# Kernel optimization log

Hardware: AMD Instinct MI355X
Metric: run time of the kernel (lower is better)

## Reference

```python
import math
import jax, jax.numpy as jnp
import numpy as np

N_HEADS = 12
D_EMBED = 768
BATCH = 2
SEQ = 2048


def setup_inputs() -> dict:
    key = jax.random.key(0)
    ks = jax.random.split(key, 5)
    scale = 0.02
    return {
        "x": jax.random.normal(ks[0], (BATCH, SEQ, D_EMBED), dtype=jnp.float32),
        "w_in": jax.random.normal(ks[1], (D_EMBED, 3 * D_EMBED), dtype=jnp.float32) * scale,
        "b_in": jax.random.normal(ks[2], (3 * D_EMBED,), dtype=jnp.float32) * scale,
        "w_out": jax.random.normal(ks[3], (D_EMBED, D_EMBED), dtype=jnp.float32) * scale,
        "b_out": jax.random.normal(ks[4], (D_EMBED,), dtype=jnp.float32) * scale,
    }


def reference(x, w_in, b_in, w_out, b_out):
    # x: [B, S, D]
    B, S, D = x.shape
    H = N_HEADS
    dh = D // H
    # Fused QKV projection: [B, S, 3D]
    qkv = x @ w_in + b_in
    q, k, v = jnp.split(qkv, 3, axis=-1)
    # [B, S, D] -> [B, H, S, dh]
    def to_heads(t):
        return t.reshape(B, S, H, dh).transpose(0, 2, 1, 3)
    q, k, v = to_heads(q), to_heads(k), to_heads(v)
    # Scaled dot-product attention (non-causal, masked=False default)
    scale = 1.0 / math.sqrt(dh)
    scores = jnp.einsum("bhqd,bhkd->bhqk", q, k) * scale  # [B, H, S, S]
    probs = jax.nn.softmax(scores, axis=-1)
    out = jnp.einsum("bhqk,bhkd->bhqd", probs, v)  # [B, H, S, dh]
    # Merge heads: [B, S, D]
    out = out.transpose(0, 2, 1, 3).reshape(B, S, D)
    return out @ w_out + b_out
```

## Files before the change

kernel.cpp:

```cpp
#include <hip/hip_runtime.h>
#include <stdint.h>

#define B_   2
#define S_   2048
#define D_   768
#define H_   12
#define DH_  64
#define N3_  2304
#define M_   4096

typedef __attribute__((ext_vector_type(8))) short    bf16x8;
typedef __attribute__((ext_vector_type(4))) float    f32x4;
typedef __attribute__((ext_vector_type(4))) int      i32x4;
typedef __attribute__((ext_vector_type(4))) unsigned short u16x4;
typedef _Float16 f16x4 __attribute__((ext_vector_type(4)));
typedef __fp16   h16x2 __attribute__((ext_vector_type(2)));

#define KSCALE 0.18033688011112042f

__device__ inline unsigned short f2bf(float f) {
    union { float f; unsigned u; } v; v.f = f;
    unsigned r = v.u + 0x7FFFu + ((v.u >> 16) & 1u);
    return (unsigned short)(r >> 16);
}

__device__ inline void async_copy16(const void* g, void* l) {
    __builtin_amdgcn_global_load_lds((const __attribute__((address_space(1))) void*)g,
                                     (__attribute__((address_space(3))) void*)l, 16, 0, 0);
}

__global__ void cvt_bf16(const float* __restrict__ in, unsigned short* __restrict__ out, int n4) {
    int i = blockIdx.x * blockDim.x + threadIdx.x;
    if (i >= n4) return;
    f32x4 v = *(const f32x4*)(in + (size_t)i * 4);
    u16x4 o;
    o.x = f2bf(v.x); o.y = f2bf(v.y); o.z = f2bf(v.z); o.w = f2bf(v.w);
    *(u16x4*)(out + (size_t)i * 4) = o;
}

__global__ void transpose_bf16(const float* __restrict__ in, unsigned short* __restrict__ out,
                               int R, int C) {
    __shared__ unsigned short t[32][33];
    int c0 = blockIdx.x * 32, r0 = blockIdx.y * 32;
    int tx = threadIdx.x, ty = threadIdx.y;
#pragma unroll
    for (int j = 0; j < 4; j++)
        t[ty + j * 8][tx] = f2bf(in[(size_t)(r0 + ty + j * 8) * C + c0 + tx]);
    __syncthreads();
#pragma unroll
    for (int j = 0; j < 4; j++)
        out[(size_t)(c0 + ty + j * 8) * R + r0 + tx] = t[tx][ty + j * 8];
}

__global__ void vtrans(const unsigned short* __restrict__ V, unsigned short* __restrict__ Vt) {
    __shared__ unsigned short t[64 * 65];
    const int bid = blockIdx.x;
    const int bh  = bid >> 5;
    const int s0  = (bid & 31) * 64;
    const int tid = threadIdx.x;
    const unsigned short* src = V  + (size_t)bh * S_ * DH_ + (size_t)s0 * DH_;
    unsigned short*       dst = Vt + (size_t)bh * DH_ * S_ + s0;
#pragma unroll
    for (int p = 0; p < 2; p++) {
        int c = p * 256 + tid;
        int s = c >> 3, dc = c & 7;
        i32x4 v = *(const i32x4*)&src[s * 64 + dc * 8];
        const unsigned short* e = (const unsigned short*)&v;
#pragma unroll
        for (int j = 0; j < 8; j++) t[(dc * 8 + j) * 65 + s] = e[j];
    }
    __syncthreads();
#pragma unroll
    for (int p = 0; p < 2; p++) {
        int c = p * 256 + tid;
        int d = c >> 3, sc = c & 7;
        unsigned short tmp[8];
#pragma unroll
        for (int j = 0; j < 8; j++) tmp[j] = t[d * 65 + sc * 8 + j];
        *(i32x4*)&dst[(size_t)d * S_ + sc * 8] = *(const i32x4*)tmp;
    }
}

template <int MODE>
__global__ __launch_bounds__(256) void gemm_bf16(
    const unsigned short* __restrict__ A,
    const unsigned short* __restrict__ Bt,
    const float* __restrict__ bias,
    void* __restrict__ Cout,
    unsigned short* __restrict__ Vnat,
    int M, int N, int K)
{
    __shared__ __align__(16) short Al[128 * 32];
    __shared__ __align__(16) short Bl[128 * 32];

    const int tid  = threadIdx.x;
    const int w    = tid >> 6;
    const int lane = tid & 63;
    const int r    = lane & 15;
    const int quad = lane >> 4;
    const int m0   = blockIdx.y * 128;
    const int n0   = blockIdx.x * 128;
    const int wm   = (w & 1) * 64;
    const int wn   = (w >> 1) * 64;

    f32x4 acc[4][4];
#pragma unroll
    for (int i = 0; i < 4; i++)
#pragma unroll
        for (int j = 0; j < 4; j++) acc[i][j] = f32x4{0.f, 0.f, 0.f, 0.f};

    const int c0 = tid, c1 = tid + 256;
    const size_t ga0 = (size_t)(m0 + (c0 >> 2)) * K + (c0 & 3) * 8;
    const size_t ga1 = (size_t)(m0 + (c1 >> 2)) * K + (c1 & 3) * 8;
    const size_t gb0 = (size_t)(n0 + (c0 >> 2)) * K + (c0 & 3) * 8;
    const size_t gb1 = (size_t)(n0 + (c1 >> 2)) * K + (c1 & 3) * 8;
    short* lA0 = &Al[(0 * 256 + w * 64) * 8];
    short* lA1 = &Al[(1 * 256 + w * 64) * 8];
    short* lB0 = &Bl[(0 * 256 + w * 64) * 8];
    short* lB1 = &Bl[(1 * 256 + w * 64) * 8];

    for (int k0 = 0; k0 < K; k0 += 32) {
        __syncthreads();
        async_copy16(A  + ga0 + k0, lA0);
        async_copy16(A  + ga1 + k0, lA1);
        async_copy16(Bt + gb0 + k0, lB0);
        async_copy16(Bt + gb1 + k0, lB1);
        __syncthreads();

        bf16x8 af[4], bf[4];
#pragma unroll
        for (int mi = 0; mi < 4; mi++)
            af[mi] = *(const bf16x8*)&Al[(wm + mi * 16 + r) * 32 + quad * 8];
#pragma unroll
        for (int ni = 0; ni < 4; ni++)
            bf[ni] = *(const bf16x8*)&Bl[(wn + ni * 16 + r) * 32 + quad * 8];
#pragma unroll
        for (int mi = 0; mi < 4; mi++)
#pragma unroll
            for (int ni = 0; ni < 4; ni++)
                acc[mi][ni] = __builtin_amdgcn_mfma_f32_16x16x32_bf16(
                    af[mi], bf[ni], acc[mi][ni], 0, 0, 0);
    }

    if (MODE == 0) {
        unsigned short* Q = (unsigned short*)Cout;
        const size_t one = (size_t)B_ * H_ * S_ * DH_;
#pragma unroll
        for (int ni = 0; ni < 4; ni++) {
            int col  = n0 + wn + ni * 16 + r;
            float bv = bias[col];
            int part = col / 768;
            int cc   = col - part * 768;
            int h    = cc >> 6;
            int d    = cc & 63;
            float scl = (part == 1) ? KSCALE : 1.0f;
            unsigned short* dst = (part == 2) ? Vnat : (Q + (size_t)part * one);
#pragma unroll
            for (int mi = 0; mi < 4; mi++) {
#pragma unroll
                for (int i = 0; i < 4; i++) {
                    int row = m0 + wm + mi * 16 + quad * 4 + i;
                    int b   = row >> 11;
                    int s   = row & 2047;
                    float v = (acc[mi][ni][i] + bv) * scl;
                    unsigned short bits;
                    if (part == 2) {
                        union { _Float16 h; unsigned short s; } cv;
                        cv.h = (_Float16)v;
                        bits = cv.s;
                    } else {
                        bits = f2bf(v);
                    }
                    dst[(((size_t)(b * H_ + h)) * S_ + s) * DH_ + d] = bits;
                }
            }
        }
    } else {
        float* Cf = (float*)Cout;
#pragma unroll
        for (int ni = 0; ni < 4; ni++) {
            int col  = n0 + wn + ni * 16 + r;
            float bv = bias[col];
#pragma unroll
            for (int mi = 0; mi < 4; mi++) {
#pragma unroll
                for (int i = 0; i < 4; i++) {
                    int row = m0 + wm + mi * 16 + quad * 4 + i;
                    Cf[(size_t)row * N + col] = acc[mi][ni][i] + bv;
                }
            }
        }
    }
}

__global__ __launch_bounds__(256) void attn_kernel(
    const unsigned short* __restrict__ Q,
    const unsigned short* __restrict__ K,
    const unsigned short* __restrict__ Vt,
    unsigned short* __restrict__ Out)
{
    __shared__ __align__(16) short Kl[64 * 64];
    __shared__ __align__(16) short Vl[64 * 64];

    const int tid  = threadIdx.x;
    const int w    = tid >> 6;
    const int lane = tid & 63;
    const int r    = lane & 15;
    const int quad = lane >> 4;
    const int xk   = r & 7;
    const int bid  = blockIdx.x;
    const int bh   = bid % 24;
    const int qb   = bid / 24;
    const int b    = bh / H_;
    const int h    = bh - b * H_;
    const size_t baseQK = (size_t)bh * S_ * DH_;
    const size_t baseV  = (size_t)bh * DH_ * S_;
    const int q0   = qb * 128;

    bf16x8 qf[2][2];
#pragma unroll
    for (int qt = 0; qt < 2; qt++) {
        const unsigned short* qp =
            Q + baseQK + (size_t)(q0 + w * 32 + qt * 16 + r) * DH_ + quad * 8;
        qf[qt][0] = *(const bf16x8*)(qp);
        qf[qt][1] = *(const bf16x8*)(qp + 32);
    }

    f32x4 o[2][4];
    f32x4 lacc[2];
#pragma unroll
    for (int qt = 0; qt < 2; qt++) {
        lacc[qt] = f32x4{0.f, 0.f, 0.f, 0.f};
#pragma unroll
        for (int nb = 0; nb < 4; nb++) o[qt][nb] = f32x4{0.f, 0.f, 0.f, 0.f};
    }

    const f16x4 ONES = {(_Float16)1.f, (_Float16)1.f, (_Float16)1.f, (_Float16)1.f};

    const int srw = tid >> 3, schk = tid & 7;
    const unsigned short* kg = K  + baseQK + tid * 8;
    const unsigned short* vg = Vt + baseV + (size_t)srw * S_ + schk * 8;
    const int lb = srw * 64 + (schk ^ (srw & 7)) * 8;

    i32x4 kreg[2], vreg[2];
    kreg[0] = *(const i32x4*)(kg);
    kreg[1] = *(const i32x4*)(kg + 2048);
    vreg[0] = *(const i32x4*)(vg);
    vreg[1] = *(const i32x4*)(vg + 32 * S_);

    for (int kt = 0; kt < 32; kt++) {
        __syncthreads();
        *(i32x4*)&Kl[lb]        = kreg[0];
        *(i32x4*)&Kl[lb + 2048] = kreg[1];
        *(i32x4*)&Vl[lb]        = vreg[0];
        *(i32x4*)&Vl[lb + 2048] = vreg[1];
        __syncthreads();

        if (kt != 31) {
            const unsigned short* kn = kg + (kt + 1) * 4096;
            const unsigned short* vn = vg + (kt + 1) * 64;
            kreg[0] = *(const i32x4*)(kn);
            kreg[1] = *(const i32x4*)(kn + 2048);
            vreg[0] = *(const i32x4*)(vn);
            vreg[1] = *(const i32x4*)(vn + 32 * S_);
        }

        f32x4 sa[2][4];
#pragma unroll
        for (int qt = 0; qt < 2; qt++)
#pragma unroll
            for (int kb = 0; kb < 4; kb++) sa[qt][kb] = f32x4{0.f, 0.f, 0.f, 0.f};
#pragma unroll
        for (int t = 0; t < 2; t++)
#pragma unroll
            for (int kb = 0; kb < 4; kb++) {
                bf16x8 kf = *(const bf16x8*)&Kl[(kb * 16 + r) * 64 + ((t * 4 + quad) ^ xk) * 8];
#pragma unroll
                for (int qt = 0; qt < 2; qt++)
                    sa[qt][kb] = __builtin_amdgcn_mfma_f32_16x16x32_bf16(
                        kf, qf[qt][t], sa[qt][kb], 0, 0, 0);
            }

        f16x4 pf[2][4];
#pragma unroll
        for (int qt = 0; qt < 2; qt++)
#pragma unroll
            for (int kb = 0; kb < 4; kb++) {
                float p0 = __builtin_amdgcn_exp2f(sa[qt][kb][0]);
                float p1 = __builtin_amdgcn_exp2f(sa[qt][kb][1]);
                float p2 = __builtin_amdgcn_exp2f(sa[qt][kb][2]);
                float p3 = __builtin_amdgcn_exp2f(sa[qt][kb][3]);
                union { f16x4 v; h16x2 h[2]; } u;
                u.h[0] = __builtin_amdgcn_cvt_pkrtz(p0, p1);
                u.h[1] = __builtin_amdgcn_cvt_pkrtz(p2, p3);
                pf[qt][kb] = u.v;
            }

#pragma unroll
        for (int kb = 0; kb < 4; kb++) {
#pragma unroll
            for (int nb = 0; nb < 4; nb++) {
                f16x4 vf = *(const f16x4*)&Vl[(nb * 16 + r) * 64 +
                                              ((kb * 2 + (quad >> 1)) ^ xk) * 8 + (quad & 1) * 4];
#pragma unroll
                for (int qt = 0; qt < 2; qt++)
                    o[qt][nb] = __builtin_amdgcn_mfma_f32_16x16x16f16(
                        pf[qt][kb], vf, o[qt][nb], 0, 0, 0);
            }
#pragma unroll
            for (int qt = 0; qt < 2; qt++)
                lacc[qt] = __builtin_amdgcn_mfma_f32_16x16x16f16(
                    pf[qt][kb], ONES, lacc[qt], 0, 0, 0);
        }
    }

#pragma unroll
    for (int qt = 0; qt < 2; qt++)
#pragma unroll
        for (int i = 0; i < 4; i++) {
            float inv = 1.0f / lacc[qt][i];
            int s = q0 + w * 32 + qt * 16 + quad * 4 + i;
            size_t ob = ((size_t)b * S_ + s) * D_ + h * DH_;
#pragma unroll
            for (int nb = 0; nb < 4; nb++)
                Out[ob + nb * 16 + r] = f2bf(o[qt][nb][i] * inv);
        }
}

extern "C" void kernel_launch(void* const* d_in, const int* in_sizes, int n_in,
                              void* d_out, int out_size, void* d_ws, size_t ws_size,
                              hipStream_t stream) {
    const float* x     = (const float*)d_in[0];
    const float* w_in  = (const float*)d_in[1];
    const float* b_in  = (const float*)d_in[2];
    const float* w_out = (const float*)d_in[3];
    const float* b_out = (const float*)d_in[4];
    float* out = (float*)d_out;
    char* ws = (char*)d_ws;

    unsigned short* xb    = (unsigned short*)(ws);
    unsigned short* winT  = (unsigned short*)(ws + 6291456);
    unsigned short* woutT = (unsigned short*)(ws + 9830400);
    unsigned short* QKV   = (unsigned short*)(ws + 11010048);
    unsigned short* tmpV  = (unsigned short*)(ws + 29884416);

    const size_t one = (size_t)B_ * H_ * S_ * DH_;
    unsigned short* Vtbuf  = QKV + 2 * one;
    unsigned short* attnO  = xb;

    cvt_bf16<<<3072, 256, 0, stream>>>(x, xb, (M_ * D_) / 4);
    transpose_bf16<<<dim3(N3_ / 32, D_ / 32), dim3(32, 8), 0, stream>>>(w_in, winT, D_, N3_);
    transpose_bf16<<<dim3(D_ / 32, D_ / 32), dim3(32, 8), 0, stream>>>(w_out, woutT, D_, D_);

    gemm_bf16<0><<<dim3(N3_ / 128, M_ / 128), 256, 0, stream>>>(
        xb, winT, b_in, (void*)QKV, tmpV, M_, N3_, D_);

    vtrans<<<24 * 32, 256, 0, stream>>>(tmpV, Vtbuf);

    attn_kernel<<<24 * (S_ / 128), 256, 0, stream>>>(
        QKV, QKV + one, Vtbuf, attnO);

    gemm_bf16<1><<<dim3(D_ / 128, M_ / 128), 256, 0, stream>>>(
        attnO, woutT, b_out, (void*)out, nullptr, M_, D_, D_);
}
```

Baseline: 184.9 us.

## Split attention key range across two blocks and combine partial outputs

Each attention block now handles half of the key sequence, which doubles the grid from 384 to 768 blocks. The aim is to fix the poor wave quantization against the GPU's CU count. Each half writes unnormalized fp16 partial outputs plus its row sums to scratch buffers that reuse existing workspace regions. A new combine kernel then adds the two halves, normalizes, and writes the bf16 head-merged layout. In exchange it adds an extra kernel launch and extra global memory traffic, and the unnormalized fp16 intermediates carry a risk of range or precision loss.

```diff
diff --git a/kernel.cpp b/kernel.cpp
--- a/kernel.cpp
+++ b/kernel.cpp
@@ -197,7 +197,9 @@
     const unsigned short* __restrict__ Q,
     const unsigned short* __restrict__ K,
     const unsigned short* __restrict__ Vt,
-    unsigned short* __restrict__ Out)
+    unsigned short* __restrict__ On0,
+    unsigned short* __restrict__ On1,
+    float* __restrict__ lbuf)
 {
     __shared__ __align__(16) short Kl[64 * 64];
     __shared__ __align__(16) short Vl[64 * 64];
@@ -210,12 +212,13 @@
     const int xk   = r & 7;
     const int bid  = blockIdx.x;
     const int bh   = bid % 24;
-    const int qb   = bid / 24;
-    const int b    = bh / H_;
-    const int h    = bh - b * H_;
+    const int t2   = bid / 24;
+    const int qb   = t2 & 15;
+    const int half = t2 >> 4;
     const size_t baseQK = (size_t)bh * S_ * DH_;
     const size_t baseV  = (size_t)bh * DH_ * S_;
     const int q0   = qb * 128;
+    const int kt0  = half * 16;
 
     bf16x8 qf[2][2];
 #pragma unroll
@@ -238,8 +241,8 @@
     const f16x4 ONES = {(_Float16)1.f, (_Float16)1.f, (_Float16)1.f, (_Float16)1.f};
 
     const int srw = tid >> 3, schk = tid & 7;
-    const unsigned short* kg = K  + baseQK + tid * 8;
-    const unsigned short* vg = Vt + baseV + (size_t)srw * S_ + schk * 8;
+    const unsigned short* kg = K  + baseQK + (size_t)kt0 * 4096 + tid * 8;
+    const unsigned short* vg = Vt + baseV + (size_t)kt0 * 64 + (size_t)srw * S_ + schk * 8;
     const int lb = srw * 64 + (schk ^ (srw & 7)) * 8;
 
     i32x4 kreg[2], vreg[2];
@@ -248,7 +251,7 @@
     vreg[0] = *(const i32x4*)(vg);
     vreg[1] = *(const i32x4*)(vg + 32 * S_);
 
-    for (int kt = 0; kt < 32; kt++) {
+    for (int it = 0; it < 16; it++) {
         __syncthreads();
         *(i32x4*)&Kl[lb]        = kreg[0];
         *(i32x4*)&Kl[lb + 2048] = kreg[1];
@@ -256,9 +259,9 @@
         *(i32x4*)&Vl[lb + 2048] = vreg[1];
         __syncthreads();
 
-        if (kt != 31) {
-            const unsigned short* kn = kg + (kt + 1) * 4096;
-            const unsigned short* vn = vg + (kt + 1) * 64;
+        if (it != 15) {
+            const unsigned short* kn = kg + (it + 1) * 4096;
+            const unsigned short* vn = vg + (it + 1) * 64;
             kreg[0] = *(const i32x4*)(kn);
             kreg[1] = *(const i32x4*)(kn + 2048);
             vreg[0] = *(const i32x4*)(vn);
@@ -314,17 +317,44 @@
         }
     }
 
+    unsigned short* Ob = half ? On1 : On0;
 #pragma unroll
     for (int qt = 0; qt < 2; qt++)
 #pragma unroll
         for (int i = 0; i < 4; i++) {
-            float inv = 1.0f / lacc[qt][i];
             int s = q0 + w * 32 + qt * 16 + quad * 4 + i;
-            size_t ob = ((size_t)b * S_ + s) * D_ + h * DH_;
-#pragma unroll
-            for (int nb = 0; nb < 4; nb++)
-                Out[ob + nb * 16 + r] = f2bf(o[qt][nb][i] * inv);
+            size_t row = (size_t)bh * S_ + s;
+            if (r == 0) lbuf[half * (24 * S_) + row] = lacc[qt][i];
+#pragma unroll
+            for (int nb = 0; nb < 4; nb++) {
+                union { _Float16 h; unsigned short u; } cv;
+                cv.h = (_Float16)o[qt][nb][i];
+                Ob[row * 64 + nb * 16 + r] = cv.u;
+            }
         }
+}
+
+__global__ void combine_attn(const unsigned short* __restrict__ On0,
+                             const unsigned short* __restrict__ On1,
+                             const float* __restrict__ lbuf,
+                             unsigned short* __restrict__ Out)
+{
+    int g   = blockIdx.x * 256 + threadIdx.x;
+    int hd8 = g % 96;
+    int bs  = g / 96;
+    int h   = hd8 >> 3;
+    int d8  = (hd8 & 7) * 8;
+    size_t row = ((size_t)((bs >> 11) * H_ + h)) * S_ + (bs & 2047);
+    float inv = 1.0f / (lbuf[row] + lbuf[24 * S_ + row]);
+    i32x4 a = *(const i32x4*)&On0[row * 64 + d8];
+    i32x4 c = *(const i32x4*)&On1[row * 64 + d8];
+    const _Float16* fa = (const _Float16*)&a;
+    const _Float16* fc = (const _Float16*)&c;
+    unsigned short tmp[8];
+#pragma unroll
+    for (int j = 0; j < 8; j++)
+        tmp[j] = f2bf(((float)fa[j] + (float)fc[j]) * inv);
+    *(i32x4*)&Out[(size_t)bs * D_ + h * 64 + d8] = *(const i32x4*)tmp;
 }
 
 extern "C" void kernel_launch(void* const* d_in, const int* in_sizes, int n_in,
@@ -345,8 +375,11 @@
     unsigned short* tmpV  = (unsigned short*)(ws + 29884416);
 
     const size_t one = (size_t)B_ * H_ * S_ * DH_;
-    unsigned short* Vtbuf  = QKV + 2 * one;
-    unsigned short* attnO  = xb;
+    unsigned short* Vtbuf = QKV + 2 * one;
+    unsigned short* On0   = xb;
+    unsigned short* On1   = tmpV;
+    float*          lbuf  = (float*)winT;
+    unsigned short* attnO = QKV;
 
     cvt_bf16<<<3072, 256, 0, stream>>>(x, xb, (M_ * D_) / 4);
     transpose_bf16<<<dim3(N3_ / 32, D_ / 32), dim3(32, 8), 0, stream>>>(w_in, winT, D_, N3_);
@@ -357,8 +390,10 @@
 
     vtrans<<<24 * 32, 256, 0, stream>>>(tmpV, Vtbuf);
 
-    attn_kernel<<<24 * (S_ / 128), 256, 0, stream>>>(
-        QKV, QKV + one, Vtbuf, attnO);
+    attn_kernel<<<24 * 16 * 2, 256, 0, stream>>>(
+        QKV, QKV + one, Vtbuf, On0, On1, lbuf);
+
+    combine_attn<<<1536, 256, 0, stream>>>(On0, On1, lbuf, attnO);
 
     gemm_bf16<1><<<dim3(D_ / 128, M_ / 128), 256, 0, stream>>>(
         attnO, woutT, b_out, (void*)out, nullptr, M_, D_, D_);
```

Result: faster. 179.2 us (-3.1%).
